# Kernel tuning notes

Measured on AMD Instinct MI355X. Metric: run time of the kernel, lower is better.

## Reference

```python
import jax, jax.numpy as jnp
import numpy as np

B, C, N = 4, 128, 25000
E = 200000            # edges per graph
H, DH = 4, 32         # heads, per-head dim
OUT = H * DH          # 128
ED = 32               # edge feature dim


def setup_inputs() -> dict:
    key = jax.random.key(0)
    ks = jax.random.split(key, 16)
    s = 0.05
    return {
        'x': jax.random.normal(ks[0], (B, C, N, 1), jnp.float32),
        'edge_index': jax.random.randint(ks[1], (B, 2, E), 0, B * N, jnp.int64),
        'edge_attr': jax.random.normal(ks[2], (B * E, ED), jnp.float32),
        'Wq': jax.random.normal(ks[3], (C, OUT), jnp.float32) * s,
        'bq': jnp.zeros((OUT,), jnp.float32),
        'Wk': jax.random.normal(ks[4], (C, OUT), jnp.float32) * s,
        'bk': jnp.zeros((OUT,), jnp.float32),
        'Wv': jax.random.normal(ks[5], (C, OUT), jnp.float32) * s,
        'bv': jnp.zeros((OUT,), jnp.float32),
        'We': jax.random.normal(ks[6], (ED, OUT), jnp.float32) * s,
        'Wskip': jax.random.normal(ks[7], (C, OUT), jnp.float32) * s,
        'bskip': jnp.zeros((OUT,), jnp.float32),
        'W1': jax.random.normal(ks[8], (OUT, 2 * OUT), jnp.float32) * s,
        'b1': jnp.zeros((2 * OUT,), jnp.float32),
        'W2': jax.random.normal(ks[9], (2 * OUT, OUT), jnp.float32) * s,
        'b2': jnp.zeros((OUT,), jnp.float32),
    }


def reference(x, edge_index, edge_attr, Wq, bq, Wk, bk, Wv, bv, We,
              Wskip, bskip, W1, b1, W2, b2):
    b, c, n, _ = x.shape
    nb = b * n
    # [B,C,N,1] -> [B*N, C]
    xf = x.squeeze(-1).transpose(0, 2, 1).reshape(nb, c)
    # [B,2,E] -> [2, B*E]
    ei = edge_index.transpose(1, 0, 2).reshape(2, -1)
    src, dst = ei[0], ei[1]

    q = (xf @ Wq + bq).reshape(nb, H, DH)
    k = (xf @ Wk + bk).reshape(nb, H, DH)
    v = (xf @ Wv + bv).reshape(nb, H, DH)
    e = (edge_attr @ We).reshape(-1, H, DH)  # [T,H,DH]

    qi = q[dst]            # gather target queries  [T,H,DH]
    kj = k[src] + e        # gather source keys + edge proj
    vj = v[src] + e

    scale = 1.0 / np.sqrt(DH).astype(np.float32)
    alpha = (qi * kj).sum(-1) * scale  # [T,H]

    # segment softmax over edges sharing a destination node
    amax = jax.ops.segment_max(alpha, dst, num_segments=nb)
    amax = jnp.where(jnp.isfinite(amax), amax, 0.0)
    ea = jnp.exp(alpha - amax[dst])
    denom = jax.ops.segment_sum(ea, dst, num_segments=nb)
    attn = ea / (denom[dst] + 1e-16)   # [T,H]

    agg = jax.ops.segment_sum(vj * attn[..., None], dst, num_segments=nb)
    out = agg.reshape(nb, OUT) + (xf @ Wskip + bskip)  # root skip

    # feed-forward + final activation
    h = jnp.maximum(out @ W1 + b1, 0.0) @ W2 + b2
    h = jnp.maximum(h, 0.0)

    # [B*N, OUT] -> [B, OUT, N, 1]
    return h.reshape(b, n, OUT).transpose(0, 2, 1)[..., None]
```

## Files before the change

kernel.cpp:

```cpp
#include <hip/hip_runtime.h>
#include <hip/hip_bf16.h>

#define NB      100000
#define NPB     25000
#define T_E     800000
#define EPG     200000
#define DMODEL  128
#define EDIM    32
#define FFD     256
#define SCAN_NBLK 98

typedef __attribute__((ext_vector_type(8))) short bf16x8;
typedef __attribute__((ext_vector_type(4))) float f32x4;
typedef __attribute__((ext_vector_type(2))) float f32x2;

__device__ inline unsigned short f2bf(float f) {
    unsigned u = __float_as_uint(f);
    unsigned r = u + 0x7fffu + ((u >> 16) & 1u);
    return (unsigned short)(r >> 16);
}
__device__ inline unsigned pack_bf16x2(float lo, float hi) {
    return (unsigned)f2bf(lo) | ((unsigned)f2bf(hi) << 16);
}
__device__ inline float bf_lo(unsigned p) { return __uint_as_float(p << 16); }
__device__ inline float bf_hi(unsigned p) { return __uint_as_float(p & 0xffff0000u); }

__global__ __launch_bounds__(256) void k_prep(
    const float* __restrict__ W1, const float* __restrict__ W2,
    const float* __restrict__ We,
    const float* __restrict__ Wq, const float* __restrict__ Wk,
    const float* __restrict__ Wv, const float* __restrict__ Wskip,
    uint4* __restrict__ w1f, uint4* __restrict__ w2f,
    uint4* __restrict__ wef, uint4* __restrict__ wpf)
{
    int t = blockIdx.x * 256 + threadIdx.x;
    int lane = t & 63;
    int frag = t >> 6;
    if (frag >= 264) return;
    int rl = lane & 15, g = lane >> 4;
    unsigned v[4];
    if (frag < 64) {
        int m1 = frag >> 2, ks = frag & 3;
        int col1 = m1 * 16 + rl;
        int k0 = ks * 32 + g * 8;
#pragma unroll
        for (int j2 = 0; j2 < 4; ++j2) {
            float f0 = W1[(k0 + 2 * j2) * FFD + col1];
            float f1 = W1[(k0 + 2 * j2 + 1) * FFD + col1];
            v[j2] = pack_bf16x2(f0, f1);
        }
        w1f[frag * 64 + lane] = make_uint4(v[0], v[1], v[2], v[3]);
    } else if (frag < 128) {
        int f2 = frag - 64;
        int m2 = f2 >> 3, ks = f2 & 7;
        int c2 = m2 * 16 + rl;
        int k0 = ks * 32 + g * 8;
#pragma unroll
        for (int j2 = 0; j2 < 4; ++j2) {
            float f0 = W2[(k0 + 2 * j2) * DMODEL + c2];
            float f1 = W2[(k0 + 2 * j2 + 1) * DMODEL + c2];
            v[j2] = pack_bf16x2(f0, f1);
        }
        w2f[f2 * 64 + lane] = make_uint4(v[0], v[1], v[2], v[3]);
    } else if (frag < 136) {
        int m = frag - 128;
        int ocol = m * 16 + rl;
        int k0 = g * 8;
#pragma unroll
        for (int j2 = 0; j2 < 4; ++j2) {
            float f0 = We[(k0 + 2 * j2) * DMODEL + ocol];
            float f1 = We[(k0 + 2 * j2 + 1) * DMODEL + ocol];
            v[j2] = pack_bf16x2(f0, f1);
        }
        wef[m * 64 + lane] = make_uint4(v[0], v[1], v[2], v[3]);
    } else {
        int fi = frag - 136;
        int m  = fi >> 5;
        int r  = fi & 31;
        int ct = r >> 2, ks = r & 3;
        const float* W = (m == 0) ? Wq : (m == 1) ? Wk : (m == 2) ? Wv : Wskip;
        int col = ct * 16 + rl;
        int k0  = ks * 32 + g * 8;
#pragma unroll
        for (int j2 = 0; j2 < 4; ++j2) {
            float f0 = W[(k0 + 2 * j2) * DMODEL + col];
            float f1 = W[(k0 + 2 * j2 + 1) * DMODEL + col];
            v[j2] = pack_bf16x2(f0, f1);
        }
        wpf[fi * 64 + lane] = make_uint4(v[0], v[1], v[2], v[3]);
    }
}

__global__ __launch_bounds__(256) void k_proj2(
    const float* __restrict__ x, const uint4* __restrict__ wpf,
    const float* __restrict__ bq, const float* __restrict__ bk,
    const float* __restrict__ bv, const float* __restrict__ bskip,
    unsigned short* __restrict__ qb16, unsigned short* __restrict__ kb16,
    unsigned short* __restrict__ vb16, unsigned short* __restrict__ skipb16)
{
    __shared__ __align__(16) char lds[32768];
    const int tid   = threadIdx.x;
    const int node0 = blockIdx.x * 128;

    {
        const int nl   = tid & 127;
        const int half = tid >> 7;
        const int node = node0 + nl;
        const bool valid = node < NB;
        int b  = node / NPB;
        int nn = node - b * NPB;
        const float* xbase = x + (size_t)b * DMODEL * NPB + nn;
#pragma unroll
        for (int o = 0; o < 8; ++o) {
            int c0 = (o * 2 + half) * 8;
            unsigned vals[4];
#pragma unroll
            for (int j2 = 0; j2 < 4; ++j2) {
                float f0 = valid ? xbase[(size_t)(c0 + 2 * j2) * NPB] : 0.f;
                float f1 = valid ? xbase[(size_t)(c0 + 2 * j2 + 1) * NPB] : 0.f;
                vals[j2] = pack_bf16x2(f0, f1);
            }
            int byte = nl * 256 + ((c0 * 2) ^ ((nl & 7) << 4));
            *(uint4*)(&lds[byte]) = make_uint4(vals[0], vals[1], vals[2], vals[3]);
        }
    }
    __syncthreads();

    const int w = tid >> 6, lane = tid & 63;
    const int rl = lane & 15, g = lane >> 4;

    const uint4* wf = wpf + (size_t)w * 32 * 64;
    const float* bi = (w == 0) ? bq : (w == 1) ? bk : (w == 2) ? bv : bskip;
    unsigned short* outp = (w == 0) ? qb16 : (w == 1) ? kb16 : (w == 2) ? vb16 : skipb16;

#pragma unroll
    for (int ct = 0; ct < 8; ++ct) {
        bf16x8 A[4];
#pragma unroll
        for (int ks = 0; ks < 4; ++ks)
            A[ks] = *(const bf16x8*)&wf[(ct * 4 + ks) * 64 + lane];
        const int colb = ct * 16 + g * 4;
        const float bb0 = bi[colb], bb1 = bi[colb + 1],
                    bb2 = bi[colb + 2], bb3 = bi[colb + 3];
#pragma unroll
        for (int nt = 0; nt < 8; ++nt) {
            const int nl = nt * 16 + rl;
            f32x4 acc = {0.f, 0.f, 0.f, 0.f};
#pragma unroll
            for (int ks = 0; ks < 4; ++ks) {
                bf16x8 B = *(const bf16x8*)(&lds[nl * 256 +
                              ((ks * 64 + g * 16) ^ ((nl & 7) << 4))]);
                acc = __builtin_amdgcn_mfma_f32_16x16x32_bf16(A[ks], B, acc, 0, 0, 0);
            }
            const int node = node0 + nl;
            if (node < NB) {
                unsigned lo = pack_bf16x2(acc[0] + bb0, acc[1] + bb1);
                unsigned hi = pack_bf16x2(acc[2] + bb2, acc[3] + bb3);
                *(uint2*)&outp[(size_t)node * DMODEL + colb] = make_uint2(lo, hi);
            }
        }
    }
}

__global__ __launch_bounds__(256) void k_hist(
    const int* __restrict__ eidx, int* __restrict__ counts)
{
    int t = blockIdx.x * 256 + threadIdx.x;
    if (t < T_E) {
        int b = t / EPG, e = t - b * EPG;
        int dst = eidx[(size_t)(b * 2 + 1) * EPG + e];
        atomicAdd(&counts[dst], 1);
    }
}

__global__ __launch_bounds__(1024) void k_scan1(
    const int* __restrict__ counts, int* __restrict__ row_start,
    int* __restrict__ bsum)
{
    __shared__ int s[1024];
    const int tid = threadIdx.x;
    const int gid = blockIdx.x * 1024 + tid;
    int v = (gid < NB) ? counts[gid] : 0;
    s[tid] = v;
    __syncthreads();
#pragma unroll
    for (int off = 1; off < 1024; off <<= 1) {
        int tv = (tid >= off) ? s[tid - off] : 0;
        __syncthreads();
        s[tid] += tv;
        __syncthreads();
    }
    int incl = s[tid];
    if (gid < NB) row_start[gid] = incl - v;
    if (tid == 1023) bsum[blockIdx.x] = incl;
}

__global__ __launch_bounds__(128) void k_scan2(int* __restrict__ bsum)
{
    __shared__ int s[128];
    const int tid = threadIdx.x;
    int v = (tid < SCAN_NBLK) ? bsum[tid] : 0;
    s[tid] = v;
    __syncthreads();
#pragma unroll
    for (int off = 1; off < 128; off <<= 1) {
        int tv = (tid >= off) ? s[tid - off] : 0;
        __syncthreads();
        s[tid] += tv;
        __syncthreads();
    }
    if (tid < SCAN_NBLK) bsum[tid] = s[tid] - v;
}

__global__ __launch_bounds__(1024) void k_scan3(
    int* __restrict__ row_start, const int* __restrict__ bsum,
    int* __restrict__ cursor)
{
    const int gid = blockIdx.x * 1024 + threadIdx.x;
    if (gid < NB) {
        int v = row_start[gid] + bsum[blockIdx.x];
        row_start[gid] = v;
        cursor[gid] = v;
    }
}

__global__ __launch_bounds__(256) void k_scatter(
    const int* __restrict__ eidx, int* __restrict__ cursor,
    int2* __restrict__ elist2)
{
    int t = blockIdx.x * 256 + threadIdx.x;
    if (t < T_E) {
        int b = t / EPG, e = t - b * EPG;
        int dst = eidx[(size_t)(b * 2 + 1) * EPG + e];
        int src = eidx[(size_t)(b * 2) * EPG + e];
        int pos = atomicAdd(&cursor[dst], 1);
        elist2[pos] = make_int2(src, t);
    }
}

__global__ __launch_bounds__(256) void k_eproj(
    const float* __restrict__ eattr, const uint4* __restrict__ wef,
    unsigned char* __restrict__ eb)
{
    const int tid = threadIdx.x;
    const int w = tid >> 6, lane = tid & 63;
    const int rl = lane & 15, g = lane >> 4;

    bf16x8 a[8];
#pragma unroll
    for (int m = 0; m < 8; ++m) a[m] = *(const bf16x8*)&wef[m * 64 + lane];

    const int nwaves = gridDim.x * 4;
    for (int tile = blockIdx.x * 4 + w; tile < T_E / 16; tile += nwaves) {
        const float* ep = &eattr[((size_t)tile * 16 + rl) * EDIM + g * 8];
        float4 f0 = *(const float4*)ep;
        float4 f1 = *(const float4*)(ep + 4);
        uint4 bu = make_uint4(pack_bf16x2(f0.x, f0.y), pack_bf16x2(f0.z, f0.w),
                              pack_bf16x2(f1.x, f1.y), pack_bf16x2(f1.z, f1.w));
        bf16x8 b = *(bf16x8*)&bu;
        f32x4 z = {0.f, 0.f, 0.f, 0.f};
        f32x4 acc[8];
#pragma unroll
        for (int m = 0; m < 8; ++m)
            acc[m] = __builtin_amdgcn_mfma_f32_16x16x32_bf16(a[m], b, z, 0, 0, 0);
        unsigned char* out = &eb[((size_t)tile * 16 + rl) * DMODEL + g * 4];
#pragma unroll
        for (int m = 0; m < 8; ++m) {
            unsigned d = __builtin_amdgcn_cvt_pk_fp8_f32(acc[m][0], acc[m][1], 0, false);
            d = __builtin_amdgcn_cvt_pk_fp8_f32(acc[m][2], acc[m][3], d, true);
            *(unsigned*)(out + m * 16) = d;
        }
    }
}

__global__ __launch_bounds__(256) void k_aggr3(
    unsigned short* qx,
    const unsigned short* __restrict__ kb16,
    const unsigned short* __restrict__ vb16,
    const unsigned short* __restrict__ skipb16,
    const unsigned char* __restrict__ eb,
    const int2* __restrict__ elist2,
    const int* __restrict__ row_start, const int* __restrict__ row_end)
{
    const int tid = threadIdx.x;
    const int w = tid >> 6, l = tid & 63;
    const int q4 = l >> 4;
    const int li = l & 15;
    const int c0 = li * 8;

    const int nwaves = gridDim.x * 4;
    for (int node = blockIdx.x * 4 + w; node < NB; node += nwaves) {
        const int rs = row_start[node];
        const int re = row_end[node];
        uint4 qp = *(const uint4*)&qx[(size_t)node * DMODEL + c0];
        const float q0 = bf_lo(qp.x), q1 = bf_hi(qp.x);
        const float q2 = bf_lo(qp.y), q3 = bf_hi(qp.y);
        const float q4_ = bf_lo(qp.z), q5 = bf_hi(qp.z);
        const float q6 = bf_lo(qp.w), q7 = bf_hi(qp.w);
        float a0 = 0.f, a1 = 0.f, a2 = 0.f, a3 = 0.f;
        float a4 = 0.f, a5 = 0.f, a6 = 0.f, a7 = 0.f, den = 0.f;

        for (int j0 = rs; j0 < re; j0 += 4) {
            const int jc = j0 + q4;
            const bool act = jc < re;
            const int jj = act ? jc : re - 1;
            int2 se = elist2[jj];
            uint4 kp = *(const uint4*)&kb16[(size_t)se.x * DMODEL + c0];
            uint4 vp = *(const uint4*)&vb16[(size_t)se.x * DMODEL + c0];
            uint2 ep8 = *(const uint2*)&eb[(size_t)se.y * DMODEL + c0];
            f32x2 exl = __builtin_amdgcn_cvt_pk_f32_fp8(ep8.x, false);
            f32x2 exh = __builtin_amdgcn_cvt_pk_f32_fp8(ep8.x, true);
            f32x2 eyl = __builtin_amdgcn_cvt_pk_f32_fp8(ep8.y, false);
            f32x2 eyh = __builtin_amdgcn_cvt_pk_f32_fp8(ep8.y, true);
            const float e0 = exl[0], e1 = exl[1], e2 = exh[0], e3 = exh[1];
            const float e4 = eyl[0], e5 = eyl[1], e6 = eyh[0], e7 = eyh[1];
            const float k0 = bf_lo(kp.x) + e0, k1 = bf_hi(kp.x) + e1;
            const float k2 = bf_lo(kp.y) + e2, k3 = bf_hi(kp.y) + e3;
            const float k4 = bf_lo(kp.z) + e4, k5 = bf_hi(kp.z) + e5;
            const float k6 = bf_lo(kp.w) + e6, k7 = bf_hi(kp.w) + e7;
            float p = q0 * k0 + q1 * k1 + q2 * k2 + q3 * k3
                    + q4_ * k4 + q5 * k5 + q6 * k6 + q7 * k7;
            p += __shfl_xor(p, 1, 64);
            p += __shfl_xor(p, 2, 64);
            float ea = act ? __expf(p * 0.17677669529663689f) : 0.f;
            a0 += ea * (bf_lo(vp.x) + e0);
            a1 += ea * (bf_hi(vp.x) + e1);
            a2 += ea * (bf_lo(vp.y) + e2);
            a3 += ea * (bf_hi(vp.y) + e3);
            a4 += ea * (bf_lo(vp.z) + e4);
            a5 += ea * (bf_hi(vp.z) + e5);
            a6 += ea * (bf_lo(vp.w) + e6);
            a7 += ea * (bf_hi(vp.w) + e7);
            den += ea;
        }
#pragma unroll
        for (int off = 16; off <= 32; off <<= 1) {
            a0 += __shfl_xor(a0, off, 64);
            a1 += __shfl_xor(a1, off, 64);
            a2 += __shfl_xor(a2, off, 64);
            a3 += __shfl_xor(a3, off, 64);
            a4 += __shfl_xor(a4, off, 64);
            a5 += __shfl_xor(a5, off, 64);
            a6 += __shfl_xor(a6, off, 64);
            a7 += __shfl_xor(a7, off, 64);
            den += __shfl_xor(den, off, 64);
        }
        float r = 1.0f / (den + 1e-16f);
        if (q4 == 0) {
            uint4 sp = *(const uint4*)&skipb16[(size_t)node * DMODEL + c0];
            uint4 o;
            o.x = pack_bf16x2(a0 * r + bf_lo(sp.x), a1 * r + bf_hi(sp.x));
            o.y = pack_bf16x2(a2 * r + bf_lo(sp.y), a3 * r + bf_hi(sp.y));
            o.z = pack_bf16x2(a4 * r + bf_lo(sp.z), a5 * r + bf_hi(sp.z));
            o.w = pack_bf16x2(a6 * r + bf_lo(sp.w), a7 * r + bf_hi(sp.w));
            *(uint4*)&qx[(size_t)node * DMODEL + c0] = o;
        }
    }
}

#define H1_OFF 16384

__global__ __launch_bounds__(256) void k_ffn_mfma(
    const unsigned short* __restrict__ xs16,
    const uint4* __restrict__ w1f, const float* __restrict__ b1,
    const uint4* __restrict__ w2f, const float* __restrict__ b2,
    float* __restrict__ out)
{
    __shared__ __align__(16) char lds[49152];
    const int tid   = threadIdx.x;
    const int node0 = blockIdx.x * 64;

#pragma unroll
    for (int i = 0; i < 4; ++i) {
        int linear = i * 256 + tid;
        int row = linear >> 4;
        int c8  = (linear & 15) * 8;
        int node = node0 + row;
        uint4 vv = (node < NB) ? *(const uint4*)&xs16[(size_t)node * DMODEL + c8]
                               : make_uint4(0, 0, 0, 0);
        int byte = row * 256 + ((c8 * 2) ^ ((row & 7) << 4));
        *(uint4*)(&lds[byte]) = vv;
    }
    __syncthreads();

    const int w = tid >> 6, lane = tid & 63;
    const int rl = lane & 15, g = lane >> 4;

    {
        f32x4 acc[4][4] = {};
#pragma unroll
        for (int ks = 0; ks < 4; ++ks) {
            bf16x8 a[4], b[4];
#pragma unroll
            for (int mt = 0; mt < 4; ++mt) {
                int m1 = w * 4 + mt;
                a[mt] = *(const bf16x8*)&w1f[(m1 * 4 + ks) * 64 + lane];
            }
#pragma unroll
            for (int nt = 0; nt < 4; ++nt) {
                int node = nt * 16 + rl;
                int byte = node * 256 + ((ks * 64 + g * 16) ^ ((node & 7) << 4));
                b[nt] = *(const bf16x8*)&lds[byte];
            }
#pragma unroll
            for (int mt = 0; mt < 4; ++mt)
#pragma unroll
                for (int nt = 0; nt < 4; ++nt)
                    acc[mt][nt] = __builtin_amdgcn_mfma_f32_16x16x32_bf16(
                        a[mt], b[nt], acc[mt][nt], 0, 0, 0);
        }
#pragma unroll
        for (int mt = 0; mt < 4; ++mt) {
            int col1_0 = w * 64 + mt * 16 + g * 4;
            float bb0 = b1[col1_0], bb1 = b1[col1_0 + 1],
                  bb2 = b1[col1_0 + 2], bb3 = b1[col1_0 + 3];
#pragma unroll
            for (int nt = 0; nt < 4; ++nt) {
                int node = nt * 16 + rl;
                float v0 = fmaxf(acc[mt][nt][0] + bb0, 0.f);
                float v1 = fmaxf(acc[mt][nt][1] + bb1, 0.f);
                float v2 = fmaxf(acc[mt][nt][2] + bb2, 0.f);
                float v3 = fmaxf(acc[mt][nt][3] + bb3, 0.f);
                unsigned lo = pack_bf16x2(v0, v1), hi = pack_bf16x2(v2, v3);
                int byte = H1_OFF + node * 512 + ((col1_0 * 2) ^ ((node & 7) << 4));
                *(uint2*)(&lds[byte]) = make_uint2(lo, hi);
            }
        }
    }
    __syncthreads();

    {
        f32x4 acc[2][4] = {};
#pragma unroll
        for (int ks = 0; ks < 8; ++ks) {
            bf16x8 a[2], b[4];
#pragma unroll
            for (int mt = 0; mt < 2; ++mt) {
                int m2 = w * 2 + mt;
                a[mt] = *(const bf16x8*)&w2f[(m2 * 8 + ks) * 64 + lane];
            }
#pragma unroll
            for (int nt = 0; nt < 4; ++nt) {
                int node = nt * 16 + rl;
                int byte = H1_OFF + node * 512 + ((ks * 64 + g * 16) ^ ((node & 7) << 4));
                b[nt] = *(const bf16x8*)&lds[byte];
            }
#pragma unroll
            for (int mt = 0; mt < 2; ++mt)
#pragma unroll
                for (int nt = 0; nt < 4; ++nt)
                    acc[mt][nt] = __builtin_amdgcn_mfma_f32_16x16x32_bf16(
                        a[mt], b[nt], acc[mt][nt], 0, 0, 0);
        }
#pragma unroll
        for (int mt = 0; mt < 2; ++mt) {
            int c2_0 = w * 32 + mt * 16 + g * 4;
#pragma unroll
            for (int nt = 0; nt < 4; ++nt) {
                int node = node0 + nt * 16 + rl;
                if (node < NB) {
                    int bb = node / NPB;
                    int nn = node - bb * NPB;
                    size_t base = (size_t)(bb * DMODEL) * NPB + nn;
#pragma unroll
                    for (int r = 0; r < 4; ++r) {
                        float v = fmaxf(acc[mt][nt][r] + b2[c2_0 + r], 0.f);
                        out[base + (size_t)(c2_0 + r) * NPB] = v;
                    }
                }
            }
        }
    }
}

extern "C" void kernel_launch(void* const* d_in, const int* in_sizes, int n_in,
                              void* d_out, int out_size, void* d_ws, size_t ws_size,
                              hipStream_t stream)
{
    const float* x     = (const float*)d_in[0];
    const int*   eidx  = (const int*)  d_in[1];
    const float* eattr = (const float*)d_in[2];
    const float* Wq    = (const float*)d_in[3];
    const float* bq    = (const float*)d_in[4];
    const float* Wk    = (const float*)d_in[5];
    const float* bk    = (const float*)d_in[6];
    const float* Wv    = (const float*)d_in[7];
    const float* bv    = (const float*)d_in[8];
    const float* We    = (const float*)d_in[9];
    const float* Wskip = (const float*)d_in[10];
    const float* bskip = (const float*)d_in[11];
    const float* W1    = (const float*)d_in[12];
    const float* b1    = (const float*)d_in[13];
    const float* W2    = (const float*)d_in[14];
    const float* b2    = (const float*)d_in[15];
    float* out = (float*)d_out;

    const size_t NBD = (size_t)NB * DMODEL;
    unsigned short* qb16    = (unsigned short*)d_ws;
    unsigned short* kb16    = qb16 + NBD;
    unsigned short* vb16    = kb16 + NBD;
    unsigned short* skipb16 = vb16 + NBD;
    unsigned char*  eb      = (unsigned char*)(skipb16 + NBD);
    uint4* w1f = (uint4*)(eb + (size_t)T_E * DMODEL);
    uint4* w2f = w1f + 64 * 64;
    uint4* wef = w2f + 64 * 64;
    uint4* wpf = wef + 8 * 64;
    int* counts    = (int*)(wpf + 128 * 64);
    int* row_start = counts + NB;
    int* cursor    = row_start + NB;
    int2* elist2   = (int2*)(cursor + NB);
    int* bsum      = (int*)(elist2 + T_E);

    hipMemsetAsync(counts, 0, NB * sizeof(int), stream);
    k_prep<<<66, 256, 0, stream>>>(W1, W2, We, Wq, Wk, Wv, Wskip,
                                   w1f, w2f, wef, wpf);
    k_proj2<<<(NB + 127) / 128, 256, 0, stream>>>(x, wpf, bq, bk, bv, bskip,
                                                  qb16, kb16, vb16, skipb16);
    k_hist<<<(T_E + 255) / 256, 256, 0, stream>>>(eidx, counts);
    k_scan1<<<SCAN_NBLK, 1024, 0, stream>>>(counts, row_start, bsum);
    k_scan2<<<1, 128, 0, stream>>>(bsum);
    k_scan3<<<SCAN_NBLK, 1024, 0, stream>>>(row_start, bsum, cursor);
    k_scatter<<<(T_E + 255) / 256, 256, 0, stream>>>(eidx, cursor, elist2);
    k_eproj<<<2048, 256, 0, stream>>>(eattr, wef, eb);
    k_aggr3<<<2048, 256, 0, stream>>>(qb16, kb16, vb16, skipb16, eb, elist2,
                                      row_start, cursor);
    k_ffn_mfma<<<(NB + 63) / 64, 256, 0, stream>>>(qb16, w1f, b1, w2f, b2, out);
}
```

Before: 369.4 us.

## Interleave K and V rows into one buffer and predicate inactive edge gathers

K and V projections are now stored interleaved per node (256-element rows), so each gathered source node's K and V sit in adjacent memory, which should improve locality for the random gathers in the aggregation kernel. Inactive tail lanes in the edge loop now skip their loads instead of reloading the last edge. The projection kernel also handles 64 nodes per block instead of 128, halving LDS and doubling the grid. The larger block count adds some scheduling overhead, and the per-wave row stride adds a little index arithmetic.

```diff
diff --git a/kernel.cpp b/kernel.cpp
--- a/kernel.cpp
+++ b/kernel.cpp
@@ -95,24 +95,24 @@
     const float* __restrict__ x, const uint4* __restrict__ wpf,
     const float* __restrict__ bq, const float* __restrict__ bk,
     const float* __restrict__ bv, const float* __restrict__ bskip,
-    unsigned short* __restrict__ qb16, unsigned short* __restrict__ kb16,
-    unsigned short* __restrict__ vb16, unsigned short* __restrict__ skipb16)
-{
-    __shared__ __align__(16) char lds[32768];
+    unsigned short* __restrict__ qb16, unsigned short* __restrict__ kvb,
+    unsigned short* __restrict__ skipb16)
+{
+    __shared__ __align__(16) char lds[16384];
     const int tid   = threadIdx.x;
-    const int node0 = blockIdx.x * 128;
+    const int node0 = blockIdx.x * 64;
 
     {
-        const int nl   = tid & 127;
-        const int half = tid >> 7;
+        const int nl   = tid & 63;
+        const int half = tid >> 6;
         const int node = node0 + nl;
         const bool valid = node < NB;
         int b  = node / NPB;
         int nn = node - b * NPB;
         const float* xbase = x + (size_t)b * DMODEL * NPB + nn;
 #pragma unroll
-        for (int o = 0; o < 8; ++o) {
-            int c0 = (o * 2 + half) * 8;
+        for (int o = 0; o < 4; ++o) {
+            int c0 = (half * 4 + o) * 8;
             unsigned vals[4];
 #pragma unroll
             for (int j2 = 0; j2 < 4; ++j2) {
@@ -131,7 +131,9 @@
 
     const uint4* wf = wpf + (size_t)w * 32 * 64;
     const float* bi = (w == 0) ? bq : (w == 1) ? bk : (w == 2) ? bv : bskip;
-    unsigned short* outp = (w == 0) ? qb16 : (w == 1) ? kb16 : (w == 2) ? vb16 : skipb16;
+    unsigned short* base = (w == 0) ? qb16 : (w == 3) ? skipb16
+                          : kvb + ((w == 2) ? 128 : 0);
+    const int rowstride = (w == 1 || w == 2) ? 256 : 128;
 
 #pragma unroll
     for (int ct = 0; ct < 8; ++ct) {
@@ -143,7 +145,7 @@
         const float bb0 = bi[colb], bb1 = bi[colb + 1],
                     bb2 = bi[colb + 2], bb3 = bi[colb + 3];
 #pragma unroll
-        for (int nt = 0; nt < 8; ++nt) {
+        for (int nt = 0; nt < 4; ++nt) {
             const int nl = nt * 16 + rl;
             f32x4 acc = {0.f, 0.f, 0.f, 0.f};
 #pragma unroll
@@ -156,7 +158,7 @@
             if (node < NB) {
                 unsigned lo = pack_bf16x2(acc[0] + bb0, acc[1] + bb1);
                 unsigned hi = pack_bf16x2(acc[2] + bb2, acc[3] + bb3);
-                *(uint2*)&outp[(size_t)node * DMODEL + colb] = make_uint2(lo, hi);
+                *(uint2*)&base[(size_t)node * rowstride + colb] = make_uint2(lo, hi);
             }
         }
     }
@@ -275,8 +277,7 @@
 
 __global__ __launch_bounds__(256) void k_aggr3(
     unsigned short* qx,
-    const unsigned short* __restrict__ kb16,
-    const unsigned short* __restrict__ vb16,
+    const unsigned short* __restrict__ kvb,
     const unsigned short* __restrict__ skipb16,
     const unsigned char* __restrict__ eb,
     const int2* __restrict__ elist2,
@@ -303,11 +304,14 @@
         for (int j0 = rs; j0 < re; j0 += 4) {
             const int jc = j0 + q4;
             const bool act = jc < re;
-            const int jj = act ? jc : re - 1;
-            int2 se = elist2[jj];
-            uint4 kp = *(const uint4*)&kb16[(size_t)se.x * DMODEL + c0];
-            uint4 vp = *(const uint4*)&vb16[(size_t)se.x * DMODEL + c0];
-            uint2 ep8 = *(const uint2*)&eb[(size_t)se.y * DMODEL + c0];
+            uint4 kp = make_uint4(0, 0, 0, 0), vp = make_uint4(0, 0, 0, 0);
+            uint2 ep8 = make_uint2(0, 0);
+            if (act) {
+                int2 se = elist2[jc];
+                kp = *(const uint4*)&kvb[(size_t)se.x * 256 + c0];
+                vp = *(const uint4*)&kvb[(size_t)se.x * 256 + 128 + c0];
+                ep8 = *(const uint2*)&eb[(size_t)se.y * DMODEL + c0];
+            }
             f32x2 exl = __builtin_amdgcn_cvt_pk_f32_fp8(ep8.x, false);
             f32x2 exh = __builtin_amdgcn_cvt_pk_f32_fp8(ep8.x, true);
             f32x2 eyl = __builtin_amdgcn_cvt_pk_f32_fp8(ep8.y, false);
@@ -497,9 +501,8 @@
 
     const size_t NBD = (size_t)NB * DMODEL;
     unsigned short* qb16    = (unsigned short*)d_ws;
-    unsigned short* kb16    = qb16 + NBD;
-    unsigned short* vb16    = kb16 + NBD;
-    unsigned short* skipb16 = vb16 + NBD;
+    unsigned short* kvb     = qb16 + NBD;
+    unsigned short* skipb16 = kvb + 2 * NBD;
     unsigned char*  eb      = (unsigned char*)(skipb16 + NBD);
     uint4* w1f = (uint4*)(eb + (size_t)T_E * DMODEL);
     uint4* w2f = w1f + 64 * 64;
@@ -514,15 +517,15 @@
     hipMemsetAsync(counts, 0, NB * sizeof(int), stream);
     k_prep<<<66, 256, 0, stream>>>(W1, W2, We, Wq, Wk, Wv, Wskip,
                                    w1f, w2f, wef, wpf);
-    k_proj2<<<(NB + 127) / 128, 256, 0, stream>>>(x, wpf, bq, bk, bv, bskip,
-                                                  qb16, kb16, vb16, skipb16);
+    k_proj2<<<(NB + 63) / 64, 256, 0, stream>>>(x, wpf, bq, bk, bv, bskip,
+                                                qb16, kvb, skipb16);
     k_hist<<<(T_E + 255) / 256, 256, 0, stream>>>(eidx, counts);
     k_scan1<<<SCAN_NBLK, 1024, 0, stream>>>(counts, row_start, bsum);
     k_scan2<<<1, 128, 0, stream>>>(bsum);
     k_scan3<<<SCAN_NBLK, 1024, 0, stream>>>(row_start, bsum, cursor);
     k_scatter<<<(T_E + 255) / 256, 256, 0, stream>>>(eidx, cursor, elist2);
     k_eproj<<<2048, 256, 0, stream>>>(eattr, wef, eb);
-    k_aggr3<<<2048, 256, 0, stream>>>(qb16, kb16, vb16, skipb16, eb, elist2,
+    k_aggr3<<<2048, 256, 0, stream>>>(qb16, kvb, skipb16, eb, elist2,
                                       row_start, cursor);
     k_ffn_mfma<<<(NB + 63) / 64, 256, 0, stream>>>(qb16, w1f, b1, w2f, b2, out);
 }
```

New measurement: 369.1 us. Within noise of the previous version (-0.1%).
